# Kernel optimization log

Hardware: AMD Instinct MI355X
Metric: run time of the kernel (lower is better)

Reference implementation:

```python
import jax, jax.numpy as jnp
import numpy as np

N = 10000      # nodes
E = 160000     # edges
G = 512        # graphs in batch
IN, H, OUT = 128, 512, 16
L = 4          # num_layers
EPS = 1e-5


def setup_inputs() -> dict:
    key = jax.random.key(0)
    ks = jax.random.split(key, 8)
    x = jax.random.normal(ks[0], (N, IN), dtype=jnp.float32)
    edge_index = jax.random.randint(ks[1], (2, E), 0, N)
    batch = jnp.sort(jax.random.randint(ks[2], (N,), 0, G))
    # GCNConv layer 0 (IN -> H) and layers 1..L-1 (H -> H), plus per-layer LayerNorm affine
    W0 = jax.random.normal(ks[3], (IN, H), dtype=jnp.float32) / np.float32(np.sqrt(IN))
    b0 = jnp.zeros((H,), jnp.float32)
    g0 = jnp.ones((IN,), jnp.float32)
    be0 = jnp.zeros((IN,), jnp.float32)
    Wh = jax.random.normal(ks[4], (L - 1, H, H), dtype=jnp.float32) / np.float32(np.sqrt(H))
    bh = jnp.zeros((L - 1, H), jnp.float32)
    gh = jnp.ones((L - 1, H), jnp.float32)
    beh = jnp.zeros((L - 1, H), jnp.float32)
    linW = jax.random.normal(ks[5], (H, OUT), dtype=jnp.float32) / np.float32(np.sqrt(H))
    linb = jnp.zeros((OUT,), jnp.float32)
    return dict(x=x, edge_index=edge_index, batch=batch, W0=W0, b0=b0, g0=g0, be0=be0,
                Wh=Wh, bh=bh, gh=gh, beh=beh, linW=linW, linb=linb)


def _layernorm(x, g, b):
    mu = jnp.mean(x, axis=-1, keepdims=True)
    var = jnp.var(x, axis=-1, keepdims=True)
    return (x - mu) * jax.lax.rsqrt(var + EPS) * g + b


def _gcn(x, W, b, src, dst, dinv):
    # GCNConv with self-loops: out_i = sum_{j->i} d_j^-1/2 d_i^-1/2 (xW)_j + d_i^-1 (xW)_i + b
    h = x @ W                                   # [N, H']
    coef = (dinv[src] * dinv[dst])[:, None]     # [E, 1]
    agg = jax.ops.segment_sum(h[src] * coef, dst, num_segments=N)
    agg = agg + h * (dinv * dinv)[:, None]      # self-loop term
    return agg + b


def reference(x, edge_index, batch, W0, b0, g0, be0, Wh, bh, gh, beh, linW, linb):
    src, dst = edge_index[0], edge_index[1]
    # degree with self-loops (counted on destination nodes, edge weight 1)
    deg = jax.ops.segment_sum(jnp.ones((E,), x.dtype), dst, num_segments=N) + 1.0
    dinv = jax.lax.rsqrt(deg)
    h = jax.nn.relu(_gcn(_layernorm(x, g0, be0), W0, b0, src, dst, dinv))
    for i in range(L - 1):
        h = jax.nn.relu(_gcn(_layernorm(h, gh[i], beh[i]), Wh[i], bh[i], src, dst, dinv))
    # scatter-mean pooling by graph id
    counts = jax.ops.segment_sum(jnp.ones((N,), x.dtype), batch, num_segments=G)
    pooled = jax.ops.segment_sum(h, batch, num_segments=G) / jnp.maximum(counts, 1.0)[:, None]
    return pooled @ linW + linb
```

## Files before the change

### kernel.cpp

```cpp
#include <hip/hip_runtime.h>

#define NN 10000
#define NE 160000
#define NG 512
#define DIN 128
#define DH 512
#define DOUT 16
#define NPAD 10112

typedef __bf16 bf16_t;
typedef __attribute__((ext_vector_type(8))) __bf16 bf16x8;
typedef __attribute__((ext_vector_type(2))) __bf16 bf16x2;
typedef __attribute__((ext_vector_type(4))) float f32x4;
typedef __attribute__((ext_vector_type(2))) float f32x2;

#define LNB 2500
#define DEGB ((NE + 255) / 256)
#define WTE (512 * DIN + 3 * DH * DH)
#define WTB ((WTE + 255) / 256)
#define CURB ((NN + 255) / 256)


__global__ __launch_bounds__(256) void k_prep(const float* __restrict__ x,
                                              const float* __restrict__ g0,
                                              const float* __restrict__ be0,
                                              bf16_t* __restrict__ lnx,
                                              const int* __restrict__ dst,
                                              int* __restrict__ deg,
                                              const float* __restrict__ W0,
                                              const float* __restrict__ Wh,
                                              bf16_t* __restrict__ Wt0,
                                              bf16_t* __restrict__ Wth,
                                              int* __restrict__ cursor) {
    int b = blockIdx.x;
    int tid = threadIdx.x;
    if (b < LNB) {
        int row = b * 4 + (tid >> 6);
        int lane = tid & 63;
        const float* xr = x + (size_t)row * DIN;
        float v0 = xr[lane], v1 = xr[lane + 64];
        float s = v0 + v1, s2 = v0 * v0 + v1 * v1;
#pragma unroll
        for (int off = 32; off; off >>= 1) {
            s += __shfl_xor(s, off);
            s2 += __shfl_xor(s2, off);
        }
        float mu = s * (1.f / 128.f);
        float var = s2 * (1.f / 128.f) - mu * mu;
        float r = rsqrtf(var + 1e-5f);
        bf16_t* yr = lnx + (size_t)row * DIN;
        yr[lane] = (bf16_t)((v0 - mu) * r * g0[lane] + be0[lane]);
        yr[lane + 64] = (bf16_t)((v1 - mu) * r * g0[lane + 64] + be0[lane + 64]);
    } else if (b < LNB + DEGB) {
        int e = (b - LNB) * 256 + tid;
        if (e < NE) atomicAdd(&deg[dst[e]], 1);
    } else if (b < LNB + DEGB + WTB) {
        int idx = (b - LNB - DEGB) * 256 + tid;
        if (idx < 512 * DIN) {
            int k = idx >> 9, n = idx & 511;
            Wt0[n * DIN + k] = (bf16_t)W0[idx];
        } else if (idx < WTE) {
            int j = idx - 512 * DIN;
            int l = j >> 18;
            int r2 = j & 262143;
            int k = r2 >> 9, n = r2 & 511;
            Wth[((size_t)l << 18) + n * DH + k] = (bf16_t)Wh[j];
        }
    } else {
        int i = (b - LNB - DEGB - WTB) * 256 + tid;
        if (i < NN) cursor[i] = 0;
    }
}


__global__ __launch_bounds__(1024) void k_scan(const int* __restrict__ cnt,
                                               int* __restrict__ rowptr,
                                               float* __restrict__ dinv) {
    __shared__ int part[1024];
    int tid = threadIdx.x;
    const int PER = 10;
    int base = tid * PER;
    int local[PER];
    int s = 0;
#pragma unroll
    for (int i = 0; i < PER; ++i) {
        int idx = base + i;
        int v = (idx < NN) ? cnt[idx] : 0;
        if (idx < NN) dinv[idx] = rsqrtf((float)v + 1.0f);
        local[i] = s;
        s += v;
    }
    part[tid] = s;
    __syncthreads();
    for (int off = 1; off < 1024; off <<= 1) {
        int v = (tid >= off) ? part[tid - off] : 0;
        __syncthreads();
        part[tid] += v;
        __syncthreads();
    }
    int offset = (tid > 0) ? part[tid - 1] : 0;
#pragma unroll
    for (int i = 0; i < PER; ++i) {
        int idx = base + i;
        if (idx < NN) rowptr[idx] = offset + local[i];
    }
    if (tid == 1023) rowptr[NN] = part[1023];
}

__global__ void k_fill_csr(const int* __restrict__ src, const int* __restrict__ dst,
                           const float* __restrict__ dinv, const int* __restrict__ rowptr,
                           int* __restrict__ cursor, int2* __restrict__ csr) {
    int e = blockIdx.x * blockDim.x + threadIdx.x;
    if (e >= NE) return;
    int s = src[e], d = dst[e];
    int pos = atomicAdd(&cursor[d], 1);
    csr[rowptr[d] + pos] = make_int2(s, __float_as_int(dinv[s] * dinv[d]));
}


__global__ __launch_bounds__(256) void k_ln512(const bf16_t* __restrict__ x,
                                               const float* __restrict__ g,
                                               const float* __restrict__ b,
                                               bf16_t* __restrict__ y) {
    int row = blockIdx.x * 4 + (threadIdx.x >> 6);
    int lane = threadIdx.x & 63;
    if (row >= NN) return;
    int c0 = lane * 8;
    bf16x8 v = *(const bf16x8*)&x[(size_t)row * DH + c0];
    float f[8];
    float s = 0.f, s2 = 0.f;
#pragma unroll
    for (int i = 0; i < 8; ++i) {
        f[i] = (float)v[i];
        s += f[i];
        s2 += f[i] * f[i];
    }
#pragma unroll
    for (int off = 32; off; off >>= 1) {
        s += __shfl_xor(s, off);
        s2 += __shfl_xor(s2, off);
    }
    float mu = s * (1.f / 512.f);
    float var = s2 * (1.f / 512.f) - mu * mu;
    float r = rsqrtf(var + 1e-5f);
    f32x4 g0 = *(const f32x4*)&g[c0], g1 = *(const f32x4*)&g[c0 + 4];
    f32x4 b0 = *(const f32x4*)&b[c0], b1 = *(const f32x4*)&b[c0 + 4];
    bf16x8 o;
#pragma unroll
    for (int i = 0; i < 4; ++i) {
        o[i] = (bf16_t)((f[i] - mu) * r * g0[i] + b0[i]);
        o[i + 4] = (bf16_t)((f[i + 4] - mu) * r * g1[i] + b1[i]);
    }
    *(bf16x8*)&y[(size_t)row * DH + c0] = o;
}


template <bool EPI>
__global__ __launch_bounds__(256) void k_gemm64(const bf16_t* __restrict__ A,
                                                const bf16_t* __restrict__ Bt,
                                                const float* __restrict__ bias,
                                                bf16_t* __restrict__ C, int K) {
    __shared__ bf16_t As[64 * 64];
    __shared__ bf16_t Bs[64 * 64];
    int tid = threadIdx.x;
    int lane = tid & 63, w = tid >> 6;
    int row0 = blockIdx.x * 64, col0 = blockIdx.y * 64;
    int wm = w >> 1, wn = w & 1;

    f32x4 acc[2][2];
#pragma unroll
    for (int i = 0; i < 2; ++i)
#pragma unroll
        for (int j = 0; j < 2; ++j) acc[i][j] = (f32x4){0.f, 0.f, 0.f, 0.f};

    int lr = lane >> 3;
    int lc = lane & 7;

    for (int kt = 0; kt < K; kt += 64) {
#pragma unroll
        for (int i = 0; i < 2; ++i) {
            int r = w * 16 + i * 8 + lr;
            int cg = lc ^ (r & 7);
            const bf16_t* srca = A + (size_t)(row0 + r) * K + kt + cg * 8;
            __builtin_amdgcn_global_load_lds(
                (const __attribute__((address_space(1))) void*)srca,
                (__attribute__((address_space(3))) void*)(As + (w * 16 + i * 8) * 64),
                16, 0, 0);
            const bf16_t* srcb = Bt + (size_t)(col0 + r) * K + kt + cg * 8;
            __builtin_amdgcn_global_load_lds(
                (const __attribute__((address_space(1))) void*)srcb,
                (__attribute__((address_space(3))) void*)(Bs + (w * 16 + i * 8) * 64),
                16, 0, 0);
        }
        __syncthreads();
#pragma unroll
        for (int ks = 0; ks < 2; ++ks) {
            bf16x8 af[2], bfr[2];
#pragma unroll
            for (int mi = 0; mi < 2; ++mi) {
                int mr = wm * 32 + mi * 16 + (lane & 15);
                int c = (ks * 4 + (lane >> 4)) ^ (mr & 7);
                af[mi] = *(const bf16x8*)&As[mr * 64 + c * 8];
            }
#pragma unroll
            for (int ni = 0; ni < 2; ++ni) {
                int nr = wn * 32 + ni * 16 + (lane & 15);
                int c = (ks * 4 + (lane >> 4)) ^ (nr & 7);
                bfr[ni] = *(const bf16x8*)&Bs[nr * 64 + c * 8];
            }
#pragma unroll
            for (int mi = 0; mi < 2; ++mi)
#pragma unroll
                for (int ni = 0; ni < 2; ++ni)
                    acc[mi][ni] = __builtin_amdgcn_mfma_f32_16x16x32_bf16(
                        af[mi], bfr[ni], acc[mi][ni], 0, 0, 0);
        }
        __syncthreads();
    }
#pragma unroll
    for (int mi = 0; mi < 2; ++mi)
#pragma unroll
        for (int ni = 0; ni < 2; ++ni) {
            int col = col0 + wn * 32 + ni * 16 + (lane & 15);
            float bv = EPI ? bias[col] : 0.f;
#pragma unroll
            for (int q = 0; q < 4; ++q) {
                int row = row0 + wm * 32 + mi * 16 + (lane >> 4) * 4 + q;
                float v = acc[mi][ni][q];
                if (EPI) v = fmaxf(v + bv, 0.f);
                C[(size_t)row * DH + col] = (bf16_t)v;
            }
        }
}


__global__ __launch_bounds__(256) void k_agg128(const bf16_t* __restrict__ H,
                                                const int* __restrict__ rowptr,
                                                const int2* __restrict__ csr,
                                                const float* __restrict__ dinv,
                                                bf16_t* __restrict__ out) {
    __shared__ float part[4][DIN];
    int n = blockIdx.x;
    int w = threadIdx.x >> 6, lane = threadIdx.x & 63;
    int c0 = lane * 2;
    float a0 = 0.f, a1 = 0.f;
    int s0 = rowptr[n], s1 = rowptr[n + 1];
    int k = s0 + w;
    for (; k + 4 < s1; k += 8) {
        int2 eA = csr[k], eB = csr[k + 4];
        float cA = __int_as_float(eA.y), cB = __int_as_float(eB.y);
        bf16x2 vA = *(const bf16x2*)&H[(size_t)eA.x * DIN + c0];
        bf16x2 vB = *(const bf16x2*)&H[(size_t)eB.x * DIN + c0];
        a0 += (float)vA[0] * cA + (float)vB[0] * cB;
        a1 += (float)vA[1] * cA + (float)vB[1] * cB;
    }
    if (k < s1) {
        int2 eA = csr[k];
        float cA = __int_as_float(eA.y);
        bf16x2 vA = *(const bf16x2*)&H[(size_t)eA.x * DIN + c0];
        a0 += (float)vA[0] * cA;
        a1 += (float)vA[1] * cA;
    }
    part[w][c0] = a0;
    part[w][c0 + 1] = a1;
    __syncthreads();
    if (threadIdx.x < 64) {
        int cc = threadIdx.x * 2;
        float b0 = part[0][cc] + part[1][cc] + part[2][cc] + part[3][cc];
        float b1 = part[0][cc + 1] + part[1][cc + 1] + part[2][cc + 1] + part[3][cc + 1];
        float di = dinv[n], sc = di * di;
        bf16x2 vs = *(const bf16x2*)&H[(size_t)n * DIN + cc];
        b0 += (float)vs[0] * sc;
        b1 += (float)vs[1] * sc;
        bf16x2 o;
        o[0] = (bf16_t)b0;
        o[1] = (bf16_t)b1;
        *(bf16x2*)&out[(size_t)n * DIN + cc] = o;
    }
}


template <bool DO_LN>
__global__ __launch_bounds__(256) void k_agg(const bf16_t* __restrict__ H,
                                             const int* __restrict__ rowptr,
                                             const int2* __restrict__ csr,
                                             const float* __restrict__ dinv,
                                             const float* __restrict__ bias,
                                             const float* __restrict__ gamma,
                                             const float* __restrict__ beta,
                                             bf16_t* __restrict__ out) {
    __shared__ float part[4][DH];
    __shared__ float rs[8];
    int n = blockIdx.x;
    int w = threadIdx.x >> 6, lane = threadIdx.x & 63;
    int c0 = lane * 8;
    float acc[8] = {0.f, 0.f, 0.f, 0.f, 0.f, 0.f, 0.f, 0.f};
    int s0 = rowptr[n], s1 = rowptr[n + 1];
    int k = s0 + w;
    for (; k + 4 < s1; k += 8) {
        int2 eA = csr[k], eB = csr[k + 4];
        float cA = __int_as_float(eA.y), cB = __int_as_float(eB.y);
        bf16x8 vA = *(const bf16x8*)&H[(size_t)eA.x * DH + c0];
        bf16x8 vB = *(const bf16x8*)&H[(size_t)eB.x * DH + c0];
#pragma unroll
        for (int i = 0; i < 8; ++i) acc[i] += (float)vA[i] * cA + (float)vB[i] * cB;
    }
    if (k < s1) {
        int2 eA = csr[k];
        float cA = __int_as_float(eA.y);
        bf16x8 vA = *(const bf16x8*)&H[(size_t)eA.x * DH + c0];
#pragma unroll
        for (int i = 0; i < 8; ++i) acc[i] += (float)vA[i] * cA;
    }
    *(f32x4*)&part[w][c0] = (f32x4){acc[0], acc[1], acc[2], acc[3]};
    *(f32x4*)&part[w][c0 + 4] = (f32x4){acc[4], acc[5], acc[6], acc[7]};
    __syncthreads();
    int cc = threadIdx.x * 2;
    f32x2 p0 = *(const f32x2*)&part[0][cc];
    f32x2 p1 = *(const f32x2*)&part[1][cc];
    f32x2 p2 = *(const f32x2*)&part[2][cc];
    f32x2 p3 = *(const f32x2*)&part[3][cc];
    float a0 = p0[0] + p1[0] + p2[0] + p3[0];
    float a1 = p0[1] + p1[1] + p2[1] + p3[1];
    float di = dinv[n], sc = di * di;
    bf16x2 vs = *(const bf16x2*)&H[(size_t)n * DH + cc];
    a0 += (float)vs[0] * sc;
    a1 += (float)vs[1] * sc;
    a0 = fmaxf(a0 + bias[cc], 0.f);
    a1 = fmaxf(a1 + bias[cc + 1], 0.f);
    bf16x2 o;
    if (DO_LN) {
        float s = a0 + a1, s2 = a0 * a0 + a1 * a1;
#pragma unroll
        for (int off = 32; off; off >>= 1) {
            s += __shfl_xor(s, off);
            s2 += __shfl_xor(s2, off);
        }
        if (lane == 0) {
            rs[w] = s;
            rs[4 + w] = s2;
        }
        __syncthreads();
        s = rs[0] + rs[1] + rs[2] + rs[3];
        s2 = rs[4] + rs[5] + rs[6] + rs[7];
        float mu = s * (1.f / 512.f);
        float var = s2 * (1.f / 512.f) - mu * mu;
        float r = rsqrtf(var + 1e-5f);
        o[0] = (bf16_t)((a0 - mu) * r * gamma[cc] + beta[cc]);
        o[1] = (bf16_t)((a1 - mu) * r * gamma[cc + 1] + beta[cc + 1]);
    } else {
        o[0] = (bf16_t)a0;
        o[1] = (bf16_t)a1;
    }
    *(bf16x2*)&out[(size_t)n * DH + cc] = o;
}


__global__ __launch_bounds__(256) void k_poolfin(const bf16_t* __restrict__ h,
                                                 const int* __restrict__ batch,
                                                 const float* __restrict__ linW,
                                                 const float* __restrict__ linb,
                                                 float* __restrict__ out) {
    __shared__ float pooled[DH];
    __shared__ float red[256];
    int g = blockIdx.x;
    int t = threadIdx.x;
    int lo = 0, hi = NN;
    while (lo < hi) {
        int mid = (lo + hi) >> 1;
        if (batch[mid] < g) lo = mid + 1;
        else hi = mid;
    }
    int start = lo;
    hi = NN;
    while (lo < hi) {
        int mid = (lo + hi) >> 1;
        if (batch[mid] < g + 1) lo = mid + 1;
        else hi = mid;
    }
    int end = lo;
    int c0 = t * 2;
    float a0 = 0.f, a1 = 0.f;
    for (int i = start; i < end; ++i) {
        bf16x2 v = *(const bf16x2*)&h[(size_t)i * DH + c0];
        a0 += (float)v[0];
        a1 += (float)v[1];
    }
    float inv = 1.f / fmaxf((float)(end - start), 1.0f);
    pooled[c0] = a0 * inv;
    pooled[c0 + 1] = a1 * inv;
    __syncthreads();
    int o = t & 15, c = t >> 4;
    float s = 0.f;
    int k0 = c * 32;
    for (int k = k0; k < k0 + 32; ++k) s += pooled[k] * linW[k * DOUT + o];
    red[t] = s;
    __syncthreads();
    if (t < DOUT) {
        float acc2 = 0.f;
        for (int cc = 0; cc < 16; ++cc) acc2 += red[cc * 16 + t];
        out[g * DOUT + t] = acc2 + linb[t];
    }
}


extern "C" void kernel_launch(void* const* d_in, const int* in_sizes, int n_in,
                              void* d_out, int out_size, void* d_ws, size_t ws_size,
                              hipStream_t stream) {
    const float* x = (const float*)d_in[0];
    const int* ei = (const int*)d_in[1];
    const int* batch = (const int*)d_in[2];
    const float* W0 = (const float*)d_in[3];
    const float* b0 = (const float*)d_in[4];
    const float* g0 = (const float*)d_in[5];
    const float* be0 = (const float*)d_in[6];
    const float* Wh = (const float*)d_in[7];
    const float* bh = (const float*)d_in[8];
    const float* gh = (const float*)d_in[9];
    const float* beh = (const float*)d_in[10];
    const float* linW = (const float*)d_in[11];
    const float* linb = (const float*)d_in[12];
    float* out = (float*)d_out;

    bf16_t* lnbuf = (bf16_t*)d_ws;
    bf16_t* Cbf = lnbuf + (size_t)NPAD * DH;
    bf16_t* lnx = Cbf + (size_t)NPAD * DH;
    bf16_t* aggx = lnx + (size_t)NPAD * DIN;
    bf16_t* Wt0 = aggx + (size_t)NPAD * DIN;
    bf16_t* Wth = Wt0 + 512 * DIN;
    float* dinv = (float*)(Wth + 3 * DH * DH);
    int* deg = (int*)(dinv + NN);
    int* rowptr = deg + NN;
    int* cursor = rowptr + NN + 1;
    int2* csr = (int2*)(cursor + NN + 1);

    const int* srcp = ei;
    const int* dstp = ei + NE;

    hipMemsetAsync(deg, 0, NN * sizeof(int), stream);
    k_prep<<<LNB + DEGB + WTB + CURB, 256, 0, stream>>>(x, g0, be0, lnx, dstp, deg,
                                                        W0, Wh, Wt0, Wth, cursor);
    k_scan<<<1, 1024, 0, stream>>>(deg, rowptr, dinv);
    k_fill_csr<<<(NE + 255) / 256, 256, 0, stream>>>(srcp, dstp, dinv, rowptr, cursor, csr);

    dim3 gemm_grid(NPAD / 64, DH / 64);

    k_agg128<<<NN, 256, 0, stream>>>(lnx, rowptr, csr, dinv, aggx);
    k_gemm64<true><<<gemm_grid, 256, 0, stream>>>(aggx, Wt0, b0, Cbf, DIN);
    k_ln512<<<(NN + 3) / 4, 256, 0, stream>>>(Cbf, gh + 0 * DH, beh + 0 * DH, lnbuf);

    for (int l = 0; l < 2; ++l) {
        k_gemm64<false><<<gemm_grid, 256, 0, stream>>>(lnbuf, Wth + (size_t)l * DH * DH,
                                                       nullptr, Cbf, DH);
        k_agg<true><<<NN, 256, 0, stream>>>(Cbf, rowptr, csr, dinv, bh + l * DH,
                                            gh + (l + 1) * DH, beh + (l + 1) * DH, lnbuf);
    }
    k_gemm64<false><<<gemm_grid, 256, 0, stream>>>(lnbuf, Wth + (size_t)2 * DH * DH,
                                                   nullptr, Cbf, DH);
    k_agg<false><<<NN, 256, 0, stream>>>(Cbf, rowptr, csr, dinv, bh + 2 * DH,
                                         nullptr, nullptr, lnbuf);

    k_poolfin<<<NG, 256, 0, stream>>>(lnbuf, batch, linW, linb, out);
}
```

Before: 207.4 us.

## Double-buffer GEMM LDS tiles and use wave-shuffle scan in k_scan

The 64x64 GEMM now keeps two LDS buffers and issues the global-to-LDS loads for the next K tile before computing on the current one, which removes one barrier per iteration and overlaps memory latency with MFMA work. Separately, the block-wide prefix scan in k_scan swaps the 10-step shared-memory Hillis-Steele scan, which needs many barriers, for wave-level shuffle scans plus a small per-wave partial-sum scan. Double buffering doubles the GEMM's LDS use to 32 KB per block, which may lower occupancy.

```diff
diff --git a/kernel.cpp b/kernel.cpp
--- a/kernel.cpp
+++ b/kernel.cpp
@@ -76,8 +76,8 @@
 __global__ __launch_bounds__(1024) void k_scan(const int* __restrict__ cnt,
                                                int* __restrict__ rowptr,
                                                float* __restrict__ dinv) {
-    __shared__ int part[1024];
-    int tid = threadIdx.x;
+    __shared__ int wsum[16];
+    int tid = threadIdx.x, lane = tid & 63, wid = tid >> 6;
     const int PER = 10;
     int base = tid * PER;
     int local[PER];
@@ -90,21 +90,32 @@
         local[i] = s;
         s += v;
     }
-    part[tid] = s;
-    __syncthreads();
-    for (int off = 1; off < 1024; off <<= 1) {
-        int v = (tid >= off) ? part[tid - off] : 0;
-        __syncthreads();
-        part[tid] += v;
-        __syncthreads();
-    }
-    int offset = (tid > 0) ? part[tid - 1] : 0;
+    int mysum = s;
+#pragma unroll
+    for (int off = 1; off < 64; off <<= 1) {
+        int v = __shfl_up(s, off);
+        if (lane >= off) s += v;
+    }
+    if (lane == 63) wsum[wid] = s;
+    __syncthreads();
+    if (tid < 16) {
+        int v = wsum[tid];
+#pragma unroll
+        for (int off = 1; off < 16; off <<= 1) {
+            int u = __shfl_up(v, off);
+            if (lane >= off) v += u;
+        }
+        wsum[tid] = v;
+    }
+    __syncthreads();
+    int woff = (wid > 0) ? wsum[wid - 1] : 0;
+    int excl = s - mysum + woff;
 #pragma unroll
     for (int i = 0; i < PER; ++i) {
         int idx = base + i;
-        if (idx < NN) rowptr[idx] = offset + local[i];
-    }
-    if (tid == 1023) rowptr[NN] = part[1023];
+        if (idx < NN) rowptr[idx] = excl + local[i];
+    }
+    if (tid == 1023) rowptr[NN] = excl + mysum;
 }
 
 __global__ void k_fill_csr(const int* __restrict__ src, const int* __restrict__ dst,
@@ -160,8 +171,8 @@
                                                 const bf16_t* __restrict__ Bt,
                                                 const float* __restrict__ bias,
                                                 bf16_t* __restrict__ C, int K) {
-    __shared__ bf16_t As[64 * 64];
-    __shared__ bf16_t Bs[64 * 64];
+    __shared__ bf16_t As[2][64 * 64];
+    __shared__ bf16_t Bs[2][64 * 64];
     int tid = threadIdx.x;
     int lane = tid & 63, w = tid >> 6;
     int row0 = blockIdx.x * 64, col0 = blockIdx.y * 64;
@@ -176,47 +187,59 @@
     int lr = lane >> 3;
     int lc = lane & 7;
 
-    for (int kt = 0; kt < K; kt += 64) {
-#pragma unroll
-        for (int i = 0; i < 2; ++i) {
-            int r = w * 16 + i * 8 + lr;
-            int cg = lc ^ (r & 7);
-            const bf16_t* srca = A + (size_t)(row0 + r) * K + kt + cg * 8;
-            __builtin_amdgcn_global_load_lds(
-                (const __attribute__((address_space(1))) void*)srca,
-                (__attribute__((address_space(3))) void*)(As + (w * 16 + i * 8) * 64),
-                16, 0, 0);
-            const bf16_t* srcb = Bt + (size_t)(col0 + r) * K + kt + cg * 8;
-            __builtin_amdgcn_global_load_lds(
-                (const __attribute__((address_space(1))) void*)srcb,
-                (__attribute__((address_space(3))) void*)(Bs + (w * 16 + i * 8) * 64),
-                16, 0, 0);
-        }
+#define STAGE(buf, kt)                                                                   \
+    {                                                                                    \
+        _Pragma("unroll") for (int i = 0; i < 2; ++i) {                                  \
+            int r = w * 16 + i * 8 + lr;                                                 \
+            int cg = lc ^ (r & 7);                                                       \
+            const bf16_t* srca = A + (size_t)(row0 + r) * K + (kt) + cg * 8;             \
+            __builtin_amdgcn_global_load_lds(                                            \
+                (const __attribute__((address_space(1))) void*)srca,                     \
+                (__attribute__((address_space(3))) void*)(As[buf] + (w * 16 + i * 8) * 64), \
+                16, 0, 0);                                                               \
+            const bf16_t* srcb = Bt + (size_t)(col0 + r) * K + (kt) + cg * 8;            \
+            __builtin_amdgcn_global_load_lds(                                            \
+                (const __attribute__((address_space(1))) void*)srcb,                     \
+                (__attribute__((address_space(3))) void*)(Bs[buf] + (w * 16 + i * 8) * 64), \
+                16, 0, 0);                                                               \
+        }                                                                                \
+    }
+
+#define COMPUTE(buf)                                                                     \
+    {                                                                                    \
+        _Pragma("unroll") for (int ks = 0; ks < 2; ++ks) {                               \
+            bf16x8 af[2], bfr[2];                                                        \
+            _Pragma("unroll") for (int mi = 0; mi < 2; ++mi) {                           \
+                int mr = wm * 32 + mi * 16 + (lane & 15);                                \
+                int c = (ks * 4 + (lane >> 4)) ^ (mr & 7);                               \
+                af[mi] = *(const bf16x8*)&As[buf][mr * 64 + c * 8];                      \
+            }                                                                            \
+            _Pragma("unroll") for (int ni = 0; ni < 2; ++ni) {                           \
+                int nr = wn * 32 + ni * 16 + (lane & 15);                                \
+                int c = (ks * 4 + (lane >> 4)) ^ (nr & 7);                               \
+                bfr[ni] = *(const bf16x8*)&Bs[buf][nr * 64 + c * 8];                     \
+            }                                                                            \
+            _Pragma("unroll") for (int mi = 0; mi < 2; ++mi)                             \
+                _Pragma("unroll") for (int ni = 0; ni < 2; ++ni)                         \
+                    acc[mi][ni] = __builtin_amdgcn_mfma_f32_16x16x32_bf16(               \
+                        af[mi], bfr[ni], acc[mi][ni], 0, 0, 0);                          \
+        }                                                                                \
+    }
+
+    STAGE(0, 0);
+    __syncthreads();
+    int cur = 0;
+    for (int kt = 64; kt < K; kt += 64) {
+        STAGE(cur ^ 1, kt);
+        COMPUTE(cur);
         __syncthreads();
-#pragma unroll
-        for (int ks = 0; ks < 2; ++ks) {
-            bf16x8 af[2], bfr[2];
-#pragma unroll
-            for (int mi = 0; mi < 2; ++mi) {
-                int mr = wm * 32 + mi * 16 + (lane & 15);
-                int c = (ks * 4 + (lane >> 4)) ^ (mr & 7);
-                af[mi] = *(const bf16x8*)&As[mr * 64 + c * 8];
-            }
-#pragma unroll
-            for (int ni = 0; ni < 2; ++ni) {
-                int nr = wn * 32 + ni * 16 + (lane & 15);
-                int c = (ks * 4 + (lane >> 4)) ^ (nr & 7);
-                bfr[ni] = *(const bf16x8*)&Bs[nr * 64 + c * 8];
-            }
-#pragma unroll
-            for (int mi = 0; mi < 2; ++mi)
-#pragma unroll
-                for (int ni = 0; ni < 2; ++ni)
-                    acc[mi][ni] = __builtin_amdgcn_mfma_f32_16x16x32_bf16(
-                        af[mi], bfr[ni], acc[mi][ni], 0, 0, 0);
-        }
-        __syncthreads();
-    }
+        cur ^= 1;
+    }
+    COMPUTE(cur);
+
+#undef STAGE
+#undef COMPUTE
+
 #pragma unroll
     for (int mi = 0; mi < 2; ++mi)
 #pragma unroll
```

Result: slower. 213.0 us (+2.7%).

## Split 512-wide aggregation into column slices with wave-per-node, unfuse LayerNorm

Applied to the files above, without the earlier changes.

The per-node aggregation kernel is replaced by one where each block covers four nodes for one 64-column slice. Each wave handles one node, and its four 16-lane groups stride over edges and combine results with shuffles instead of shared memory and block barriers. LayerNorm can no longer be fused because a block no longer sees a full row, so it moves to a separate k_ln512 pass through a new intermediate buffer. The aim is better cache locality per column slice and no block-level synchronisation, at the cost of an extra kernel launch and an extra write and read of the activations each layer.

```diff
diff --git a/kernel.cpp b/kernel.cpp
--- a/kernel.cpp
+++ b/kernel.cpp
@@ -10,6 +10,7 @@
 
 typedef __bf16 bf16_t;
 typedef __attribute__((ext_vector_type(8))) __bf16 bf16x8;
+typedef __attribute__((ext_vector_type(4))) __bf16 bf16x4;
 typedef __attribute__((ext_vector_type(2))) __bf16 bf16x2;
 typedef __attribute__((ext_vector_type(4))) float f32x4;
 typedef __attribute__((ext_vector_type(2))) float f32x2;
@@ -280,79 +281,55 @@
 }
 
 
-template <bool DO_LN>
-__global__ __launch_bounds__(256) void k_agg(const bf16_t* __restrict__ H,
-                                             const int* __restrict__ rowptr,
-                                             const int2* __restrict__ csr,
-                                             const float* __restrict__ dinv,
-                                             const float* __restrict__ bias,
-                                             const float* __restrict__ gamma,
-                                             const float* __restrict__ beta,
-                                             bf16_t* __restrict__ out) {
-    __shared__ float part[4][DH];
-    __shared__ float rs[8];
-    int n = blockIdx.x;
+__global__ __launch_bounds__(256) void k_agg_slice(const bf16_t* __restrict__ H,
+                                                   const int* __restrict__ rowptr,
+                                                   const int2* __restrict__ csr,
+                                                   const float* __restrict__ dinv,
+                                                   const float* __restrict__ bias,
+                                                   bf16_t* __restrict__ out) {
+    int bid = blockIdx.x;
+    int s = bid & 7;
     int w = threadIdx.x >> 6, lane = threadIdx.x & 63;
-    int c0 = lane * 8;
-    float acc[8] = {0.f, 0.f, 0.f, 0.f, 0.f, 0.f, 0.f, 0.f};
+    int n = ((bid >> 3) << 2) + w;
+    int g = lane >> 4, cl = lane & 15;
+    int c0 = s * 64 + cl * 4;
+    float a0 = 0.f, a1 = 0.f, a2 = 0.f, a3 = 0.f;
     int s0 = rowptr[n], s1 = rowptr[n + 1];
-    int k = s0 + w;
+    int k = s0 + g;
     for (; k + 4 < s1; k += 8) {
-        int2 eA = csr[k], eB = csr[k + 4];
-        float cA = __int_as_float(eA.y), cB = __int_as_float(eB.y);
-        bf16x8 vA = *(const bf16x8*)&H[(size_t)eA.x * DH + c0];
-        bf16x8 vB = *(const bf16x8*)&H[(size_t)eB.x * DH + c0];
-#pragma unroll
-        for (int i = 0; i < 8; ++i) acc[i] += (float)vA[i] * cA + (float)vB[i] * cB;
+        int2 e0 = csr[k], e1 = csr[k + 4];
+        bf16x4 v0 = *(const bf16x4*)&H[(size_t)e0.x * DH + c0];
+        bf16x4 v1 = *(const bf16x4*)&H[(size_t)e1.x * DH + c0];
+        float c0f = __int_as_float(e0.y), c1f = __int_as_float(e1.y);
+        a0 += (float)v0[0] * c0f + (float)v1[0] * c1f;
+        a1 += (float)v0[1] * c0f + (float)v1[1] * c1f;
+        a2 += (float)v0[2] * c0f + (float)v1[2] * c1f;
+        a3 += (float)v0[3] * c0f + (float)v1[3] * c1f;
     }
     if (k < s1) {
-        int2 eA = csr[k];
-        float cA = __int_as_float(eA.y);
-        bf16x8 vA = *(const bf16x8*)&H[(size_t)eA.x * DH + c0];
-#pragma unroll
-        for (int i = 0; i < 8; ++i) acc[i] += (float)vA[i] * cA;
-    }
-    *(f32x4*)&part[w][c0] = (f32x4){acc[0], acc[1], acc[2], acc[3]};
-    *(f32x4*)&part[w][c0 + 4] = (f32x4){acc[4], acc[5], acc[6], acc[7]};
-    __syncthreads();
-    int cc = threadIdx.x * 2;
-    f32x2 p0 = *(const f32x2*)&part[0][cc];
-    f32x2 p1 = *(const f32x2*)&part[1][cc];
-    f32x2 p2 = *(const f32x2*)&part[2][cc];
-    f32x2 p3 = *(const f32x2*)&part[3][cc];
-    float a0 = p0[0] + p1[0] + p2[0] + p3[0];
-    float a1 = p0[1] + p1[1] + p2[1] + p3[1];
-    float di = dinv[n], sc = di * di;
-    bf16x2 vs = *(const bf16x2*)&H[(size_t)n * DH + cc];
-    a0 += (float)vs[0] * sc;
-    a1 += (float)vs[1] * sc;
-    a0 = fmaxf(a0 + bias[cc], 0.f);
-    a1 = fmaxf(a1 + bias[cc + 1], 0.f);
-    bf16x2 o;
-    if (DO_LN) {
-        float s = a0 + a1, s2 = a0 * a0 + a1 * a1;
-#pragma unroll
-        for (int off = 32; off; off >>= 1) {
-            s += __shfl_xor(s, off);
-            s2 += __shfl_xor(s2, off);
-        }
-        if (lane == 0) {
-            rs[w] = s;
-            rs[4 + w] = s2;
-        }
-        __syncthreads();
-        s = rs[0] + rs[1] + rs[2] + rs[3];
-        s2 = rs[4] + rs[5] + rs[6] + rs[7];
-        float mu = s * (1.f / 512.f);
-        float var = s2 * (1.f / 512.f) - mu * mu;
-        float r = rsqrtf(var + 1e-5f);
-        o[0] = (bf16_t)((a0 - mu) * r * gamma[cc] + beta[cc]);
-        o[1] = (bf16_t)((a1 - mu) * r * gamma[cc + 1] + beta[cc + 1]);
-    } else {
-        o[0] = (bf16_t)a0;
-        o[1] = (bf16_t)a1;
-    }
-    *(bf16x2*)&out[(size_t)n * DH + cc] = o;
+        int2 e0 = csr[k];
+        bf16x4 v0 = *(const bf16x4*)&H[(size_t)e0.x * DH + c0];
+        float c0f = __int_as_float(e0.y);
+        a0 += (float)v0[0] * c0f;
+        a1 += (float)v0[1] * c0f;
+        a2 += (float)v0[2] * c0f;
+        a3 += (float)v0[3] * c0f;
+    }
+    a0 += __shfl_xor(a0, 16); a0 += __shfl_xor(a0, 32);
+    a1 += __shfl_xor(a1, 16); a1 += __shfl_xor(a1, 32);
+    a2 += __shfl_xor(a2, 16); a2 += __shfl_xor(a2, 32);
+    a3 += __shfl_xor(a3, 16); a3 += __shfl_xor(a3, 32);
+    if (g == 0) {
+        float di = dinv[n], sc = di * di;
+        bf16x4 vs = *(const bf16x4*)&H[(size_t)n * DH + c0];
+        f32x4 bb = *(const f32x4*)&bias[c0];
+        bf16x4 o;
+        o[0] = (bf16_t)fmaxf(a0 + (float)vs[0] * sc + bb[0], 0.f);
+        o[1] = (bf16_t)fmaxf(a1 + (float)vs[1] * sc + bb[1], 0.f);
+        o[2] = (bf16_t)fmaxf(a2 + (float)vs[2] * sc + bb[2], 0.f);
+        o[3] = (bf16_t)fmaxf(a3 + (float)vs[3] * sc + bb[3], 0.f);
+        *(bf16x4*)&out[(size_t)n * DH + c0] = o;
+    }
 }
 
 
@@ -424,7 +401,8 @@
 
     bf16_t* lnbuf = (bf16_t*)d_ws;
     bf16_t* Cbf = lnbuf + (size_t)NPAD * DH;
-    bf16_t* lnx = Cbf + (size_t)NPAD * DH;
+    bf16_t* hbuf = Cbf + (size_t)NPAD * DH;
+    bf16_t* lnx = hbuf + (size_t)NPAD * DH;
     bf16_t* aggx = lnx + (size_t)NPAD * DIN;
     bf16_t* Wt0 = aggx + (size_t)NPAD * DIN;
     bf16_t* Wth = Wt0 + 512 * DIN;
@@ -452,13 +430,15 @@
     for (int l = 0; l < 2; ++l) {
         k_gemm64<false><<<gemm_grid, 256, 0, stream>>>(lnbuf, Wth + (size_t)l * DH * DH,
                                                        nullptr, Cbf, DH);
-        k_agg<true><<<NN, 256, 0, stream>>>(Cbf, rowptr, csr, dinv, bh + l * DH,
-                                            gh + (l + 1) * DH, beh + (l + 1) * DH, lnbuf);
+        k_agg_slice<<<(NN / 4) * 8, 256, 0, stream>>>(Cbf, rowptr, csr, dinv,
+                                                      bh + l * DH, hbuf);
+        k_ln512<<<(NN + 3) / 4, 256, 0, stream>>>(hbuf, gh + (l + 1) * DH,
+                                                  beh + (l + 1) * DH, lnbuf);
     }
     k_gemm64<false><<<gemm_grid, 256, 0, stream>>>(lnbuf, Wth + (size_t)2 * DH * DH,
                                                    nullptr, Cbf, DH);
-    k_agg<false><<<NN, 256, 0, stream>>>(Cbf, rowptr, csr, dinv, bh + 2 * DH,
-                                         nullptr, nullptr, lnbuf);
-
-    k_poolfin<<<NG, 256, 0, stream>>>(lnbuf, batch, linW, linb, out);
-}
+    k_agg_slice<<<(NN / 4) * 8, 256, 0, stream>>>(Cbf, rowptr, csr, dinv,
+                                                  bh + 2 * DH, hbuf);
+
+    k_poolfin<<<NG, 256, 0, stream>>>(hbuf, batch, linW, linb, out);
+}
```

After: 253.4 us. 1.22x slower.
